# Optimization experiments

Measured on AMD Instinct MI355X. Metric: run time of the kernel, lower is better.

## Reference

```python
import jax, jax.numpy as jnp
import numpy as np

N_NODES = 50000
N_EDGES = 1600000
DIM = 128
HEADS = 8
HEAD_DIM = DIM // HEADS


def setup_inputs() -> dict:
    key = jax.random.key(0)
    ks = jax.random.split(key, 12)
    s = 1.0 / np.sqrt(DIM)
    return {
        "x": jax.random.normal(ks[0], (N_NODES, DIM), dtype=jnp.float32),
        "src": jax.random.randint(ks[1], (N_EDGES,), 0, N_NODES, dtype=jnp.int32),
        "dst": jax.random.randint(ks[2], (N_EDGES,), 0, N_NODES, dtype=jnp.int32),
        "Wq": jax.random.uniform(ks[3], (DIM, DIM), jnp.float32, -s, s),
        "bq": jax.random.uniform(ks[4], (DIM,), jnp.float32, -s, s),
        "Wk": jax.random.uniform(ks[5], (DIM, DIM), jnp.float32, -s, s),
        "bk": jax.random.uniform(ks[6], (DIM,), jnp.float32, -s, s),
        "Wv": jax.random.uniform(ks[7], (DIM, DIM), jnp.float32, -s, s),
        "bv": jax.random.uniform(ks[8], (DIM,), jnp.float32, -s, s),
        "Wo": jax.random.uniform(ks[9], (DIM, DIM), jnp.float32, -s, s),
        "bo": jax.random.uniform(ks[10], (DIM,), jnp.float32, -s, s),
    }


def reference(x, src, dst, Wq, bq, Wk, bk, Wv, bv, Wo, bo):
    # Linear projections (torch Linear: x @ W.T + b), split into heads
    q = (x @ Wq.T + bq).reshape(-1, HEADS, HEAD_DIM)  # [N, H, Dh]
    k = (x @ Wk.T + bk).reshape(-1, HEADS, HEAD_DIM)
    v = (x @ Wv.T + bv).reshape(-1, HEADS, HEAD_DIM)

    # u_dot_v: per-edge dot of q[src] and k[dst] per head -> [E, H]
    scores = jnp.einsum("ehd,ehd->eh", q[src], k[dst]) / np.sqrt(HEAD_DIM).astype(np.float32)

    # edge_softmax: softmax over edges grouped by destination node
    m = jax.ops.segment_max(scores, dst, num_segments=N_NODES)  # [N, H]
    e = jnp.exp(scores - m[dst])
    z = jax.ops.segment_sum(e, dst, num_segments=N_NODES)  # [N, H]
    probs = e / z[dst]  # [E, H]

    # u_mul_e_sum: scatter-add of v[src] * probs into dst -> [N, H, Dh]
    msg = v[src] * probs[:, :, None]
    agg = jax.ops.segment_sum(msg, dst, num_segments=N_NODES)

    out = agg.reshape(-1, DIM) @ Wo.T + bo  # dropout p=0.0 -> identity
    return out
```

## Files before the change

kernel.cpp:

```cpp
#include <hip/hip_runtime.h>
#include <hip/hip_bf16.h>
#include <math.h>

#define N_NODES 50000
#define N_EDGES 1600000
#define NBUCK 256
#define NBUCK_ACTIVE ((N_NODES + 255) / 256)
#define P1_BLOCKS ((N_EDGES + 4095) / 4096)
#define CAP 9216

typedef short bf16x8 __attribute__((ext_vector_type(8)));
typedef float f32x4 __attribute__((ext_vector_type(4)));

#define SC2 0.3606737602222409f
#define THR2 11.541560327111707f

static __device__ __forceinline__ unsigned short f2bf(float f) {
  unsigned int b = __float_as_uint(f);
  unsigned int r = (b + 0x7FFFu + ((b >> 16) & 1u)) >> 16;
  return (unsigned short)r;
}
static __device__ __forceinline__ float bf_lo(unsigned int u) {
  return __uint_as_float(u << 16);
}
static __device__ __forceinline__ float bf_hi(unsigned int u) {
  return __uint_as_float(u & 0xFFFF0000u);
}

__global__ __launch_bounds__(256) void convert_w(
    const float* __restrict__ Wq, const float* __restrict__ Wk,
    const float* __restrict__ Wv, const float* __restrict__ Wo,
    unsigned short* __restrict__ wb) {
  int idx = blockIdx.x * 256 + threadIdx.x;
  wb[idx] = f2bf(Wq[idx]);
  wb[16384 + idx] = f2bf(Wk[idx]);
  wb[32768 + idx] = f2bf(Wv[idx]);
  wb[49152 + idx] = f2bf(Wo[idx]);
}

__global__ __launch_bounds__(256) void mfma_qkv(
    const float* __restrict__ x, const unsigned short* __restrict__ wb,
    const float* __restrict__ bq, const float* __restrict__ bk,
    const float* __restrict__ bv,
    unsigned short* __restrict__ qv, unsigned short* __restrict__ kb, int nrows) {
  __shared__ __align__(16) unsigned short qvs[64 * 264];
  __shared__ __align__(16) unsigned short ks[64 * 136];
  const int tid = threadIdx.x;
  const int w = tid >> 6;
  const int lane = tid & 63;
  const int lr = lane & 15;
  const int kg = lane >> 4;
  const int rowbase = blockIdx.x * 64;
  const int wrow = rowbase + w * 16;
  const int arow = min(wrow + lr, nrows - 1);

  bf16x8 af[4];
  const float* xr = x + (size_t)arow * 128;
#pragma unroll
  for (int ksub = 0; ksub < 4; ++ksub) {
    const int k0 = ksub * 32 + kg * 8;
    float4 f0 = *(const float4*)(xr + k0);
    float4 f1 = *(const float4*)(xr + k0 + 4);
    af[ksub][0] = (short)f2bf(f0.x);
    af[ksub][1] = (short)f2bf(f0.y);
    af[ksub][2] = (short)f2bf(f0.z);
    af[ksub][3] = (short)f2bf(f0.w);
    af[ksub][4] = (short)f2bf(f1.x);
    af[ksub][5] = (short)f2bf(f1.y);
    af[ksub][6] = (short)f2bf(f1.z);
    af[ksub][7] = (short)f2bf(f1.w);
  }

  for (int p = 0; p < 3; ++p) {
    const unsigned short* wp = wb + p * 16384;
    const float* bias = (p == 0) ? bq : (p == 1) ? bk : bv;
    f32x4 acc[8];
#pragma unroll
    for (int nt = 0; nt < 8; ++nt) {
      float b = bias[nt * 16 + lr];
      acc[nt] = (f32x4){b, b, b, b};
    }
#pragma unroll
    for (int ksub = 0; ksub < 4; ++ksub) {
#pragma unroll
      for (int nt = 0; nt < 8; ++nt) {
        bf16x8 bfr = *(const bf16x8*)(wp + (size_t)(nt * 16 + lr) * 128 +
                                      ksub * 32 + kg * 8);
        acc[nt] =
            __builtin_amdgcn_mfma_f32_16x16x32_bf16(af[ksub], bfr, acc[nt], 0, 0, 0);
      }
    }
    if (p == 0) {
#pragma unroll
      for (int nt = 0; nt < 8; ++nt) {
        int col = nt * 16 + lr;
        int pos = 4 * (col >> 1) + (col & 1);
#pragma unroll
        for (int r = 0; r < 4; ++r)
          qvs[(w * 16 + kg * 4 + r) * 264 + pos] = f2bf(acc[nt][r]);
      }
    } else if (p == 1) {
#pragma unroll
      for (int nt = 0; nt < 8; ++nt) {
        int col = nt * 16 + lr;
#pragma unroll
        for (int r = 0; r < 4; ++r)
          ks[(w * 16 + kg * 4 + r) * 136 + col] = f2bf(acc[nt][r]);
      }
    } else {
#pragma unroll
      for (int nt = 0; nt < 8; ++nt) {
        int col = nt * 16 + lr;
        int pos = 4 * (col >> 1) + (col & 1) + 2;
#pragma unroll
        for (int r = 0; r < 4; ++r)
          qvs[(w * 16 + kg * 4 + r) * 264 + pos] = f2bf(acc[nt][r]);
      }
    }
  }
  __syncthreads();
#pragma unroll
  for (int i = 0; i < 8; ++i) {
    int idx = i * 256 + tid;
    int lrow = idx >> 5;
    int u16o = (idx & 31) * 8;
    int grow = rowbase + lrow;
    if (grow < nrows)
      *(uint4*)(qv + (size_t)grow * 256 + u16o) =
          *(const uint4*)&qvs[lrow * 264 + u16o];
  }
#pragma unroll
  for (int i = 0; i < 4; ++i) {
    int idx = i * 256 + tid;
    int lrow = idx >> 4;
    int u16o = (idx & 15) * 8;
    int grow = rowbase + lrow;
    if (grow < nrows)
      *(uint4*)(kb + (size_t)grow * 128 + u16o) =
          *(const uint4*)&ks[lrow * 136 + u16o];
  }
}

__global__ __launch_bounds__(256) void mfma_out(
    const unsigned short* __restrict__ aggb, const unsigned short* __restrict__ wo,
    const float* __restrict__ bo, float* __restrict__ out, int nrows) {
  const int tid = threadIdx.x;
  const int w = tid >> 6;
  const int lane = tid & 63;
  const int lr = lane & 15;
  const int kg = lane >> 4;
  const int wrow = blockIdx.x * 64 + w * 16;
  const int arow = min(wrow + lr, nrows - 1);

  bf16x8 af[4];
#pragma unroll
  for (int ksub = 0; ksub < 4; ++ksub)
    af[ksub] = *(const bf16x8*)(aggb + (size_t)arow * 128 + ksub * 32 + kg * 8);

  f32x4 acc[8];
#pragma unroll
  for (int nt = 0; nt < 8; ++nt) {
    float b = bo[nt * 16 + lr];
    acc[nt] = (f32x4){b, b, b, b};
  }
#pragma unroll
  for (int ksub = 0; ksub < 4; ++ksub) {
#pragma unroll
    for (int nt = 0; nt < 8; ++nt) {
      bf16x8 bfr = *(const bf16x8*)(wo + (size_t)(nt * 16 + lr) * 128 +
                                    ksub * 32 + kg * 8);
      acc[nt] =
          __builtin_amdgcn_mfma_f32_16x16x32_bf16(af[ksub], bfr, acc[nt], 0, 0, 0);
    }
  }
#pragma unroll
  for (int nt = 0; nt < 8; ++nt) {
    int col = nt * 16 + lr;
#pragma unroll
    for (int r = 0; r < 4; ++r) {
      int grow = wrow + kg * 4 + r;
      if (grow < nrows) out[(size_t)grow * 128 + col] = acc[nt][r];
    }
  }
}

__global__ __launch_bounds__(256) void bucket_partition(
    const int* __restrict__ src, const int* __restrict__ dst,
    int* __restrict__ bcursor, unsigned int* __restrict__ packed) {
  __shared__ int h[NBUCK];
  __shared__ int gbase[NBUCK];
  const int t = threadIdx.x;
  h[t] = 0;
  __syncthreads();
  const int base = blockIdx.x * 4096;
  unsigned int val[16];
  int binrank[16];
#pragma unroll
  for (int i = 0; i < 16; ++i) {
    int e = base + i * 256 + t;
    if (e < N_EDGES) {
      int d = dst[e];
      val[i] = ((unsigned)d << 16) | (unsigned)src[e];
      int bin = d >> 8;
      int r = atomicAdd(&h[bin], 1);
      binrank[i] = (bin << 16) | r;
    } else {
      binrank[i] = -1;
    }
  }
  __syncthreads();
  if (h[t] > 0) gbase[t] = atomicAdd(&bcursor[t], h[t]);
  __syncthreads();
#pragma unroll
  for (int i = 0; i < 16; ++i) {
    if (binrank[i] >= 0) {
      int bin = binrank[i] >> 16;
      int r = binrank[i] & 0xFFFF;
      packed[(size_t)bin * CAP + gbase[bin] + r] = val[i];
    }
  }
}

__global__ __launch_bounds__(256) void bucket_finalize(
    const unsigned int* __restrict__ packed, const int* __restrict__ bcursor,
    int* __restrict__ ebeg, int* __restrict__ eend,
    unsigned short* __restrict__ ssrc) {
  __shared__ int cnt[NBUCK];
  __shared__ int sd[NBUCK];
  __shared__ int cur[NBUCK];
  const int t = threadIdx.x;
  const int b = blockIdx.x;
  const int beg = b * CAP;
  const int n_in_bucket = min(bcursor[b], CAP);
  cnt[t] = 0;
  __syncthreads();
  for (int e = t; e < n_in_bucket; e += 256)
    atomicAdd(&cnt[(packed[beg + e] >> 16) & 255], 1);
  __syncthreads();
  const int own = cnt[t];
  sd[t] = own;
  __syncthreads();
  for (int d = 1; d < NBUCK; d <<= 1) {
    int v = (t >= d) ? sd[t - d] : 0;
    __syncthreads();
    sd[t] += v;
    __syncthreads();
  }
  const int excl = sd[t] - own;
  cur[t] = excl;
  const int node = b * 256 + t;
  if (node < N_NODES) {
    ebeg[node] = beg + excl;
    eend[node] = beg + excl + own;
  }
  __syncthreads();
  for (int e = t; e < n_in_bucket; e += 256) {
    unsigned int p = packed[beg + e];
    int local = (p >> 16) & 255;
    int r = atomicAdd(&cur[local], 1);
    ssrc[beg + r] = (unsigned short)(p & 0xFFFFu);
  }
}

__global__ __launch_bounds__(256) void edge_agg_kernel(
    const unsigned short* __restrict__ qv, const unsigned short* __restrict__ kb,
    const int* __restrict__ ebeg, const int* __restrict__ eend,
    const unsigned short* __restrict__ ssrc, unsigned short* __restrict__ aggb) {
  const int wid = threadIdx.x >> 6;
  const int lane = threadIdx.x & 63;
  const int n = blockIdx.x * 4 + wid;
  if (n >= N_NODES) return;
  const int l16 = lane & 15;
  const int qq = lane >> 4;
  const int loff = l16 * 16;

  const uint4 ku = *(const uint4*)(kb + (size_t)n * 128 + l16 * 8);
  const float k0 = bf_lo(ku.x), k1 = bf_hi(ku.x), k2 = bf_lo(ku.y), k3 = bf_hi(ku.y);
  const float k4 = bf_lo(ku.z), k5 = bf_hi(ku.z), k6 = bf_lo(ku.w), k7 = bf_hi(ku.w);

  const int start = ebeg[n];
  const int end = eend[n];

  float m = -INFINITY, zz = 0.0f;
  float a0 = 0, a1 = 0, a2 = 0, a3 = 0, a4 = 0, a5 = 0, a6 = 0, a7 = 0;

  int base = start;
  for (; base + 8 <= end; base += 8) {
    int sA = ssrc[base + qq];
    int sB = ssrc[base + 4 + qq];
    const unsigned short* rA = qv + ((size_t)sA << 8) + loff;
    const unsigned short* rB = qv + ((size_t)sB << 8) + loff;
    uint4 tA0 = *(const uint4*)rA;
    uint4 tA1 = *(const uint4*)(rA + 8);
    uint4 tB0 = *(const uint4*)rB;
    uint4 tB1 = *(const uint4*)(rB + 8);
    float pA = bf_lo(tA0.x) * k0 + bf_hi(tA0.x) * k1 + bf_lo(tA0.z) * k2 +
               bf_hi(tA0.z) * k3 + bf_lo(tA1.x) * k4 + bf_hi(tA1.x) * k5 +
               bf_lo(tA1.z) * k6 + bf_hi(tA1.z) * k7;
    float pB = bf_lo(tB0.x) * k0 + bf_hi(tB0.x) * k1 + bf_lo(tB0.z) * k2 +
               bf_hi(tB0.z) * k3 + bf_lo(tB1.x) * k4 + bf_hi(tB1.x) * k5 +
               bf_lo(tB1.z) * k6 + bf_hi(tB1.z) * k7;
    pA += __shfl_xor(pA, 1);
    pB += __shfl_xor(pB, 1);
    float scA = pA * SC2;
    float scB = pB * SC2;
    float mx = fmaxf(scA, scB);
    if (!__all(mx <= m + THR2)) {
      float mn = fmaxf(m, mx);
      float r = (m == -INFINITY) ? 0.0f : __builtin_amdgcn_exp2f(m - mn);
      zz *= r;
      a0 *= r; a1 *= r; a2 *= r; a3 *= r;
      a4 *= r; a5 *= r; a6 *= r; a7 *= r;
      m = mn;
    }
    float peA = __builtin_amdgcn_exp2f(scA - m);
    float peB = __builtin_amdgcn_exp2f(scB - m);
    zz += peA + peB;
    a0 = fmaf(peA, bf_lo(tA0.y), fmaf(peB, bf_lo(tB0.y), a0));
    a1 = fmaf(peA, bf_hi(tA0.y), fmaf(peB, bf_hi(tB0.y), a1));
    a2 = fmaf(peA, bf_lo(tA0.w), fmaf(peB, bf_lo(tB0.w), a2));
    a3 = fmaf(peA, bf_hi(tA0.w), fmaf(peB, bf_hi(tB0.w), a3));
    a4 = fmaf(peA, bf_lo(tA1.y), fmaf(peB, bf_lo(tB1.y), a4));
    a5 = fmaf(peA, bf_hi(tA1.y), fmaf(peB, bf_hi(tB1.y), a5));
    a6 = fmaf(peA, bf_lo(tA1.w), fmaf(peB, bf_lo(tB1.w), a6));
    a7 = fmaf(peA, bf_hi(tA1.w), fmaf(peB, bf_hi(tB1.w), a7));
  }
  for (; base < end; base += 4) {
    int idx = base + qq;
    bool valid = idx < end;
    int s = ssrc[valid ? idx : end - 1];
    const unsigned short* rA = qv + ((size_t)s << 8) + loff;
    uint4 t0 = *(const uint4*)rA;
    uint4 t1 = *(const uint4*)(rA + 8);
    float p = bf_lo(t0.x) * k0 + bf_hi(t0.x) * k1 + bf_lo(t0.z) * k2 +
              bf_hi(t0.z) * k3 + bf_lo(t1.x) * k4 + bf_hi(t1.x) * k5 +
              bf_lo(t1.z) * k6 + bf_hi(t1.z) * k7;
    p += __shfl_xor(p, 1);
    float sc = valid ? p * SC2 : -INFINITY;
    if (!__all(sc <= m + THR2)) {
      float mn = fmaxf(m, sc);
      float r = (m == -INFINITY) ? 0.0f : __builtin_amdgcn_exp2f(m - mn);
      zz *= r;
      a0 *= r; a1 *= r; a2 *= r; a3 *= r;
      a4 *= r; a5 *= r; a6 *= r; a7 *= r;
      m = mn;
    }
    float pe = valid ? __builtin_amdgcn_exp2f(sc - m) : 0.0f;
    zz += pe;
    a0 = fmaf(pe, bf_lo(t0.y), a0);
    a1 = fmaf(pe, bf_hi(t0.y), a1);
    a2 = fmaf(pe, bf_lo(t0.w), a2);
    a3 = fmaf(pe, bf_hi(t0.w), a3);
    a4 = fmaf(pe, bf_lo(t1.y), a4);
    a5 = fmaf(pe, bf_hi(t1.y), a5);
    a6 = fmaf(pe, bf_lo(t1.w), a6);
    a7 = fmaf(pe, bf_hi(t1.w), a7);
  }

#pragma unroll
  for (int off = 16; off <= 32; off <<= 1) {
    float m2 = __shfl_xor(m, off);
    float z2 = __shfl_xor(zz, off);
    float b0 = __shfl_xor(a0, off), b1 = __shfl_xor(a1, off);
    float b2 = __shfl_xor(a2, off), b3 = __shfl_xor(a3, off);
    float b4 = __shfl_xor(a4, off), b5 = __shfl_xor(a5, off);
    float b6 = __shfl_xor(a6, off), b7 = __shfl_xor(a7, off);
    float M = fmaxf(m, m2);
    float w1 = (m == -INFINITY) ? 0.0f : __builtin_amdgcn_exp2f(m - M);
    float w2 = (m2 == -INFINITY) ? 0.0f : __builtin_amdgcn_exp2f(m2 - M);
    zz = zz * w1 + z2 * w2;
    a0 = a0 * w1 + b0 * w2; a1 = a1 * w1 + b1 * w2;
    a2 = a2 * w1 + b2 * w2; a3 = a3 * w1 + b3 * w2;
    a4 = a4 * w1 + b4 * w2; a5 = a5 * w1 + b5 * w2;
    a6 = a6 * w1 + b6 * w2; a7 = a7 * w1 + b7 * w2;
    m = M;
  }
  float inv = (zz > 0.0f) ? 1.0f / zz : 0.0f;

  if (qq == 0) {
    unsigned short o[8] = {f2bf(a0 * inv), f2bf(a1 * inv), f2bf(a2 * inv),
                           f2bf(a3 * inv), f2bf(a4 * inv), f2bf(a5 * inv),
                           f2bf(a6 * inv), f2bf(a7 * inv)};
    *(uint4*)(aggb + (size_t)n * 128 + l16 * 8) = *(const uint4*)o;
  }
}

extern "C" void kernel_launch(void* const* d_in, const int* in_sizes, int n_in,
                              void* d_out, int out_size, void* d_ws, size_t ws_size,
                              hipStream_t stream) {
  const float* x  = (const float*)d_in[0];
  const int* src  = (const int*)d_in[1];
  const int* dst  = (const int*)d_in[2];
  const float* Wq = (const float*)d_in[3];
  const float* bq = (const float*)d_in[4];
  const float* Wk = (const float*)d_in[5];
  const float* bk = (const float*)d_in[6];
  const float* Wv = (const float*)d_in[7];
  const float* bv = (const float*)d_in[8];
  const float* Wo = (const float*)d_in[9];
  const float* bo = (const float*)d_in[10];
  float* out = (float*)d_out;

  char* ws = (char*)d_ws;
  size_t off = 0;
  auto carve = [&](size_t bytes) {
    size_t r = off;
    off = (off + bytes + 255) & ~(size_t)255;
    return r;
  };
  unsigned short* qv   = (unsigned short*)(ws + carve((size_t)N_NODES * 512));
  unsigned short* kb   = (unsigned short*)(ws + carve((size_t)N_NODES * 256));
  unsigned short* aggb = (unsigned short*)(ws + carve((size_t)N_NODES * 256));
  unsigned int* packed = (unsigned int*)(ws + carve((size_t)NBUCK * CAP * 4));
  unsigned short* ssrc = (unsigned short*)(ws + carve((size_t)NBUCK * CAP * 2));
  int* ebeg    = (int*)(ws + carve((size_t)N_NODES * sizeof(int)));
  int* eend    = (int*)(ws + carve((size_t)N_NODES * sizeof(int)));
  int* bcursor = (int*)(ws + carve(NBUCK * sizeof(int)));
  unsigned short* wb = (unsigned short*)(ws + carve((size_t)4 * 128 * 128 * 2));

  hipMemsetAsync(bcursor, 0, NBUCK * sizeof(int), stream);

  convert_w<<<64, 256, 0, stream>>>(Wq, Wk, Wv, Wo, wb);

  const int gemm_grid = (N_NODES + 63) / 64;
  mfma_qkv<<<gemm_grid, 256, 0, stream>>>(x, wb, bq, bk, bv, qv, kb, N_NODES);

  bucket_partition<<<P1_BLOCKS, 256, 0, stream>>>(src, dst, bcursor, packed);
  bucket_finalize<<<NBUCK_ACTIVE, 256, 0, stream>>>(packed, bcursor, ebeg, eend,
                                                    ssrc);

  edge_agg_kernel<<<(N_NODES + 3) / 4, 256, 0, stream>>>(qv, kb, ebeg, eend,
                                                         ssrc, aggb);

  mfma_out<<<gemm_grid, 256, 0, stream>>>(aggb, wb + 3 * 16384, bo, out, N_NODES);
}
```

Measured before the change: 231.7 us.

## Split interleaved QV into separate Q/V arrays, unroll edge loop, fuse weight conversion

Q and V were stored interleaved in one 512-byte record per node. They are now written to separate 256-byte arrays, and the edge aggregation loop gathers one 16-byte Q and one 16-byte V chunk per lane, with four edges per lane per iteration instead of two. The weight bf16 conversion is folded into the bucket_partition launch, which now also reads src/dst as int4 vectors, and edge_agg gets an occupancy hint of 8 blocks. Gathers now hit two separate arrays, which may reduce locality, and the wider unroll raises register pressure.

Result: slower. 262.3 us (+13.2%).

```diff
diff --git a/kernel.cpp b/kernel.cpp
--- a/kernel.cpp
+++ b/kernel.cpp
@@ -27,24 +27,13 @@
   return __uint_as_float(u & 0xFFFF0000u);
 }
 
-__global__ __launch_bounds__(256) void convert_w(
-    const float* __restrict__ Wq, const float* __restrict__ Wk,
-    const float* __restrict__ Wv, const float* __restrict__ Wo,
-    unsigned short* __restrict__ wb) {
-  int idx = blockIdx.x * 256 + threadIdx.x;
-  wb[idx] = f2bf(Wq[idx]);
-  wb[16384 + idx] = f2bf(Wk[idx]);
-  wb[32768 + idx] = f2bf(Wv[idx]);
-  wb[49152 + idx] = f2bf(Wo[idx]);
-}
-
 __global__ __launch_bounds__(256) void mfma_qkv(
     const float* __restrict__ x, const unsigned short* __restrict__ wb,
     const float* __restrict__ bq, const float* __restrict__ bk,
     const float* __restrict__ bv,
-    unsigned short* __restrict__ qv, unsigned short* __restrict__ kb, int nrows) {
-  __shared__ __align__(16) unsigned short qvs[64 * 264];
-  __shared__ __align__(16) unsigned short ks[64 * 136];
+    unsigned short* __restrict__ qrec, unsigned short* __restrict__ kb,
+    unsigned short* __restrict__ vrec, int nrows) {
+  __shared__ __align__(16) unsigned short sbuf[64 * 136];
   const int tid = threadIdx.x;
   const int w = tid >> 6;
   const int lane = tid & 63;
@@ -74,6 +63,7 @@
   for (int p = 0; p < 3; ++p) {
     const unsigned short* wp = wb + p * 16384;
     const float* bias = (p == 0) ? bq : (p == 1) ? bk : bv;
+    unsigned short* gout = (p == 0) ? qrec : (p == 1) ? kb : vrec;
     f32x4 acc[8];
 #pragma unroll
     for (int nt = 0; nt < 8; ++nt) {
@@ -90,54 +80,25 @@
             __builtin_amdgcn_mfma_f32_16x16x32_bf16(af[ksub], bfr, acc[nt], 0, 0, 0);
       }
     }
-    if (p == 0) {
-#pragma unroll
-      for (int nt = 0; nt < 8; ++nt) {
-        int col = nt * 16 + lr;
-        int pos = 4 * (col >> 1) + (col & 1);
-#pragma unroll
-        for (int r = 0; r < 4; ++r)
-          qvs[(w * 16 + kg * 4 + r) * 264 + pos] = f2bf(acc[nt][r]);
-      }
-    } else if (p == 1) {
-#pragma unroll
-      for (int nt = 0; nt < 8; ++nt) {
-        int col = nt * 16 + lr;
-#pragma unroll
-        for (int r = 0; r < 4; ++r)
-          ks[(w * 16 + kg * 4 + r) * 136 + col] = f2bf(acc[nt][r]);
-      }
-    } else {
-#pragma unroll
-      for (int nt = 0; nt < 8; ++nt) {
-        int col = nt * 16 + lr;
-        int pos = 4 * (col >> 1) + (col & 1) + 2;
-#pragma unroll
-        for (int r = 0; r < 4; ++r)
-          qvs[(w * 16 + kg * 4 + r) * 264 + pos] = f2bf(acc[nt][r]);
-      }
-    }
-  }
-  __syncthreads();
-#pragma unroll
-  for (int i = 0; i < 8; ++i) {
-    int idx = i * 256 + tid;
-    int lrow = idx >> 5;
-    int u16o = (idx & 31) * 8;
-    int grow = rowbase + lrow;
-    if (grow < nrows)
-      *(uint4*)(qv + (size_t)grow * 256 + u16o) =
-          *(const uint4*)&qvs[lrow * 264 + u16o];
-  }
-#pragma unroll
-  for (int i = 0; i < 4; ++i) {
-    int idx = i * 256 + tid;
-    int lrow = idx >> 4;
-    int u16o = (idx & 15) * 8;
-    int grow = rowbase + lrow;
-    if (grow < nrows)
-      *(uint4*)(kb + (size_t)grow * 128 + u16o) =
-          *(const uint4*)&ks[lrow * 136 + u16o];
+    __syncthreads();
+#pragma unroll
+    for (int nt = 0; nt < 8; ++nt) {
+      int col = nt * 16 + lr;
+#pragma unroll
+      for (int r = 0; r < 4; ++r)
+        sbuf[(w * 16 + kg * 4 + r) * 136 + col] = f2bf(acc[nt][r]);
+    }
+    __syncthreads();
+#pragma unroll
+    for (int i = 0; i < 4; ++i) {
+      int idx = i * 256 + tid;
+      int lrow = idx >> 4;
+      int u16o = (idx & 15) * 8;
+      int grow = rowbase + lrow;
+      if (grow < nrows)
+        *(uint4*)(gout + (size_t)grow * 128 + u16o) =
+            *(const uint4*)&sbuf[lrow * 136 + u16o];
+    }
   }
 }
 
@@ -186,26 +147,44 @@
 
 __global__ __launch_bounds__(256) void bucket_partition(
     const int* __restrict__ src, const int* __restrict__ dst,
-    int* __restrict__ bcursor, unsigned int* __restrict__ packed) {
+    int* __restrict__ bcursor, unsigned int* __restrict__ packed,
+    const float* __restrict__ Wq, const float* __restrict__ Wk,
+    const float* __restrict__ Wv, const float* __restrict__ Wo,
+    unsigned short* __restrict__ wb) {
+  const int t = threadIdx.x;
+  if (blockIdx.x < 64) {
+    int idx = blockIdx.x * 256 + t;
+    wb[idx] = f2bf(Wq[idx]);
+    wb[16384 + idx] = f2bf(Wk[idx]);
+    wb[32768 + idx] = f2bf(Wv[idx]);
+    wb[49152 + idx] = f2bf(Wo[idx]);
+  }
+
   __shared__ int h[NBUCK];
   __shared__ int gbase[NBUCK];
-  const int t = threadIdx.x;
   h[t] = 0;
   __syncthreads();
-  const int base = blockIdx.x * 4096;
+  const int base4 = blockIdx.x * 1024;
   unsigned int val[16];
   int binrank[16];
 #pragma unroll
-  for (int i = 0; i < 16; ++i) {
-    int e = base + i * 256 + t;
-    if (e < N_EDGES) {
-      int d = dst[e];
-      val[i] = ((unsigned)d << 16) | (unsigned)src[e];
-      int bin = d >> 8;
-      int r = atomicAdd(&h[bin], 1);
-      binrank[i] = (bin << 16) | r;
+  for (int i = 0; i < 4; ++i) {
+    int i4 = base4 + i * 256 + t;
+    if (i4 < N_EDGES / 4) {
+      int4 s4 = ((const int4*)src)[i4];
+      int4 d4 = ((const int4*)dst)[i4];
+      int ss[4] = {s4.x, s4.y, s4.z, s4.w};
+      int dd[4] = {d4.x, d4.y, d4.z, d4.w};
+#pragma unroll
+      for (int j = 0; j < 4; ++j) {
+        val[i * 4 + j] = ((unsigned)dd[j] << 16) | (unsigned)ss[j];
+        int bin = dd[j] >> 8;
+        int r = atomicAdd(&h[bin], 1);
+        binrank[i * 4 + j] = (bin << 16) | r;
+      }
     } else {
-      binrank[i] = -1;
+#pragma unroll
+      for (int j = 0; j < 4; ++j) binrank[i * 4 + j] = -1;
     }
   }
   __syncthreads();
@@ -262,8 +241,9 @@
   }
 }
 
-__global__ __launch_bounds__(256) void edge_agg_kernel(
-    const unsigned short* __restrict__ qv, const unsigned short* __restrict__ kb,
+__global__ __launch_bounds__(256, 8) void edge_agg_kernel(
+    const unsigned short* __restrict__ qrec, const unsigned short* __restrict__ vrec,
+    const unsigned short* __restrict__ kb,
     const int* __restrict__ ebeg, const int* __restrict__ eend,
     const unsigned short* __restrict__ ssrc, unsigned short* __restrict__ aggb) {
   const int wid = threadIdx.x >> 6;
@@ -272,9 +252,9 @@
   if (n >= N_NODES) return;
   const int l16 = lane & 15;
   const int qq = lane >> 4;
-  const int loff = l16 * 16;
-
-  const uint4 ku = *(const uint4*)(kb + (size_t)n * 128 + l16 * 8);
+  const int loff = l16 * 8;
+
+  const uint4 ku = *(const uint4*)(kb + (size_t)n * 128 + loff);
   const float k0 = bf_lo(ku.x), k1 = bf_hi(ku.x), k2 = bf_lo(ku.y), k3 = bf_hi(ku.y);
   const float k4 = bf_lo(ku.z), k5 = bf_hi(ku.z), k6 = bf_lo(ku.w), k7 = bf_hi(ku.w);
 
@@ -284,27 +264,46 @@
   float m = -INFINITY, zz = 0.0f;
   float a0 = 0, a1 = 0, a2 = 0, a3 = 0, a4 = 0, a5 = 0, a6 = 0, a7 = 0;
 
+#define DOT8(t0, t1)                                                   \
+  (bf_lo(t0.x) * k0 + bf_hi(t0.x) * k1 + bf_lo(t0.y) * k2 +            \
+   bf_hi(t0.y) * k3 + bf_lo(t0.z) * k4 + bf_hi(t0.z) * k5 +            \
+   bf_lo(t0.w) * k6 + bf_hi(t0.w) * k7)
+
+#define ACC8(pe, tv)                        \
+  a0 = fmaf(pe, bf_lo(tv.x), a0);           \
+  a1 = fmaf(pe, bf_hi(tv.x), a1);           \
+  a2 = fmaf(pe, bf_lo(tv.y), a2);           \
+  a3 = fmaf(pe, bf_hi(tv.y), a3);           \
+  a4 = fmaf(pe, bf_lo(tv.z), a4);           \
+  a5 = fmaf(pe, bf_hi(tv.z), a5);           \
+  a6 = fmaf(pe, bf_lo(tv.w), a6);           \
+  a7 = fmaf(pe, bf_hi(tv.w), a7)
+
   int base = start;
-  for (; base + 8 <= end; base += 8) {
+  for (; base + 16 <= end; base += 16) {
     int sA = ssrc[base + qq];
     int sB = ssrc[base + 4 + qq];
-    const unsigned short* rA = qv + ((size_t)sA << 8) + loff;
-    const unsigned short* rB = qv + ((size_t)sB << 8) + loff;
-    uint4 tA0 = *(const uint4*)rA;
-    uint4 tA1 = *(const uint4*)(rA + 8);
-    uint4 tB0 = *(const uint4*)rB;
-    uint4 tB1 = *(const uint4*)(rB + 8);
-    float pA = bf_lo(tA0.x) * k0 + bf_hi(tA0.x) * k1 + bf_lo(tA0.z) * k2 +
-               bf_hi(tA0.z) * k3 + bf_lo(tA1.x) * k4 + bf_hi(tA1.x) * k5 +
-               bf_lo(tA1.z) * k6 + bf_hi(tA1.z) * k7;
-    float pB = bf_lo(tB0.x) * k0 + bf_hi(tB0.x) * k1 + bf_lo(tB0.z) * k2 +
-               bf_hi(tB0.z) * k3 + bf_lo(tB1.x) * k4 + bf_hi(tB1.x) * k5 +
-               bf_lo(tB1.z) * k6 + bf_hi(tB1.z) * k7;
+    int sC = ssrc[base + 8 + qq];
+    int sD = ssrc[base + 12 + qq];
+    const uint4 qA = *(const uint4*)(qrec + ((size_t)sA << 7) + loff);
+    const uint4 vA = *(const uint4*)(vrec + ((size_t)sA << 7) + loff);
+    const uint4 qB = *(const uint4*)(qrec + ((size_t)sB << 7) + loff);
+    const uint4 vB = *(const uint4*)(vrec + ((size_t)sB << 7) + loff);
+    const uint4 qC = *(const uint4*)(qrec + ((size_t)sC << 7) + loff);
+    const uint4 vC = *(const uint4*)(vrec + ((size_t)sC << 7) + loff);
+    const uint4 qD = *(const uint4*)(qrec + ((size_t)sD << 7) + loff);
+    const uint4 vD = *(const uint4*)(vrec + ((size_t)sD << 7) + loff);
+
+    float pA = DOT8(qA, );
+    float pB = DOT8(qB, );
+    float pC = DOT8(qC, );
+    float pD = DOT8(qD, );
     pA += __shfl_xor(pA, 1);
     pB += __shfl_xor(pB, 1);
-    float scA = pA * SC2;
-    float scB = pB * SC2;
-    float mx = fmaxf(scA, scB);
+    pC += __shfl_xor(pC, 1);
+    pD += __shfl_xor(pD, 1);
+    float scA = pA * SC2, scB = pB * SC2, scC = pC * SC2, scD = pD * SC2;
+    float mx = fmaxf(fmaxf(scA, scB), fmaxf(scC, scD));
     if (!__all(mx <= m + THR2)) {
       float mn = fmaxf(m, mx);
       float r = (m == -INFINITY) ? 0.0f : __builtin_amdgcn_exp2f(m - mn);
@@ -315,26 +314,21 @@
     }
     float peA = __builtin_amdgcn_exp2f(scA - m);
     float peB = __builtin_amdgcn_exp2f(scB - m);
-    zz += peA + peB;
-    a0 = fmaf(peA, bf_lo(tA0.y), fmaf(peB, bf_lo(tB0.y), a0));
-    a1 = fmaf(peA, bf_hi(tA0.y), fmaf(peB, bf_hi(tB0.y), a1));
-    a2 = fmaf(peA, bf_lo(tA0.w), fmaf(peB, bf_lo(tB0.w), a2));
-    a3 = fmaf(peA, bf_hi(tA0.w), fmaf(peB, bf_hi(tB0.w), a3));
-    a4 = fmaf(peA, bf_lo(tA1.y), fmaf(peB, bf_lo(tB1.y), a4));
-    a5 = fmaf(peA, bf_hi(tA1.y), fmaf(peB, bf_hi(tB1.y), a5));
-    a6 = fmaf(peA, bf_lo(tA1.w), fmaf(peB, bf_lo(tB1.w), a6));
-    a7 = fmaf(peA, bf_hi(tA1.w), fmaf(peB, bf_hi(tB1.w), a7));
+    float peC = __builtin_amdgcn_exp2f(scC - m);
+    float peD = __builtin_amdgcn_exp2f(scD - m);
+    zz += (peA + peB) + (peC + peD);
+    ACC8(peA, vA);
+    ACC8(peB, vB);
+    ACC8(peC, vC);
+    ACC8(peD, vD);
   }
   for (; base < end; base += 4) {
     int idx = base + qq;
     bool valid = idx < end;
     int s = ssrc[valid ? idx : end - 1];
-    const unsigned short* rA = qv + ((size_t)s << 8) + loff;
-    uint4 t0 = *(const uint4*)rA;
-    uint4 t1 = *(const uint4*)(rA + 8);
-    float p = bf_lo(t0.x) * k0 + bf_hi(t0.x) * k1 + bf_lo(t0.z) * k2 +
-              bf_hi(t0.z) * k3 + bf_lo(t1.x) * k4 + bf_hi(t1.x) * k5 +
-              bf_lo(t1.z) * k6 + bf_hi(t1.z) * k7;
+    const uint4 q0 = *(const uint4*)(qrec + ((size_t)s << 7) + loff);
+    const uint4 v0 = *(const uint4*)(vrec + ((size_t)s << 7) + loff);
+    float p = DOT8(q0, );
     p += __shfl_xor(p, 1);
     float sc = valid ? p * SC2 : -INFINITY;
     if (!__all(sc <= m + THR2)) {
@@ -347,15 +341,10 @@
     }
     float pe = valid ? __builtin_amdgcn_exp2f(sc - m) : 0.0f;
     zz += pe;
-    a0 = fmaf(pe, bf_lo(t0.y), a0);
-    a1 = fmaf(pe, bf_hi(t0.y), a1);
-    a2 = fmaf(pe, bf_lo(t0.w), a2);
-    a3 = fmaf(pe, bf_hi(t0.w), a3);
-    a4 = fmaf(pe, bf_lo(t1.y), a4);
-    a5 = fmaf(pe, bf_hi(t1.y), a5);
-    a6 = fmaf(pe, bf_lo(t1.w), a6);
-    a7 = fmaf(pe, bf_hi(t1.w), a7);
-  }
+    ACC8(pe, v0);
+  }
+#undef DOT8
+#undef ACC8
 
 #pragma unroll
   for (int off = 16; off <= 32; off <<= 1) {
@@ -381,7 +370,7 @@
     unsigned short o[8] = {f2bf(a0 * inv), f2bf(a1 * inv), f2bf(a2 * inv),
                            f2bf(a3 * inv), f2bf(a4 * inv), f2bf(a5 * inv),
                            f2bf(a6 * inv), f2bf(a7 * inv)};
-    *(uint4*)(aggb + (size_t)n * 128 + l16 * 8) = *(const uint4*)o;
+    *(uint4*)(aggb + (size_t)n * 128 + loff) = *(const uint4*)o;
   }
 }
 
@@ -408,7 +397,8 @@
     off = (off + bytes + 255) & ~(size_t)255;
     return r;
   };
-  unsigned short* qv   = (unsigned short*)(ws + carve((size_t)N_NODES * 512));
+  unsigned short* qrec = (unsigned short*)(ws + carve((size_t)N_NODES * 256));
+  unsigned short* vrec = (unsigned short*)(ws + carve((size_t)N_NODES * 256));
   unsigned short* kb   = (unsigned short*)(ws + carve((size_t)N_NODES * 256));
   unsigned short* aggb = (unsigned short*)(ws + carve((size_t)N_NODES * 256));
   unsigned int* packed = (unsigned int*)(ws + carve((size_t)NBUCK * CAP * 4));
@@ -420,17 +410,18 @@
 
   hipMemsetAsync(bcursor, 0, NBUCK * sizeof(int), stream);
 
-  convert_w<<<64, 256, 0, stream>>>(Wq, Wk, Wv, Wo, wb);
+  bucket_partition<<<P1_BLOCKS, 256, 0, stream>>>(src, dst, bcursor, packed,
+                                                  Wq, Wk, Wv, Wo, wb);
 
   const int gemm_grid = (N_NODES + 63) / 64;
-  mfma_qkv<<<gemm_grid, 256, 0, stream>>>(x, wb, bq, bk, bv, qv, kb, N_NODES);
-
-  bucket_partition<<<P1_BLOCKS, 256, 0, stream>>>(src, dst, bcursor, packed);
+  mfma_qkv<<<gemm_grid, 256, 0, stream>>>(x, wb, bq, bk, bv, qrec, kb, vrec,
+                                          N_NODES);
+
   bucket_finalize<<<NBUCK_ACTIVE, 256, 0, stream>>>(packed, bcursor, ebeg, eend,
                                                     ssrc);
 
-  edge_agg_kernel<<<(N_NODES + 3) / 4, 256, 0, stream>>>(qv, kb, ebeg, eend,
-                                                         ssrc, aggb);
+  edge_agg_kernel<<<(N_NODES + 3) / 4, 256, 0, stream>>>(qrec, vrec, kb, ebeg,
+                                                         eend, ssrc, aggb);
 
   mfma_out<<<gemm_grid, 256, 0, stream>>>(aggb, wb + 3 * 16384, bo, out, N_NODES);
 }
```
